# Optimization experiments

Hardware: AMD Instinct MI355X
Metric: run time of the kernel (lower is better)

## Reference

```python
import jax, jax.numpy as jnp
import numpy as np

B, T, C_IN = 2, 4096, 1024
INTER, OUT = 1024, 1024
ROPE_DIM = 64
GAMMA = 0.99609375  # 1 - 2**-8
GROUPS = 32
EPS = 1e-6


def setup_inputs() -> dict:
    key = jax.random.key(0)
    k = jax.random.split(key, 4)
    return {
        "X_Q": jax.random.normal(k[0], (B, T, C_IN), dtype=jnp.float32),
        "W_Q": jax.random.normal(k[1], (C_IN, INTER), dtype=jnp.float32) / C_IN,
        "W_K": jax.random.normal(k[2], (C_IN, INTER), dtype=jnp.float32) / C_IN,
        "W_V": jax.random.normal(k[3], (C_IN, OUT), dtype=jnp.float32) / C_IN,
        "gn_weight": jnp.ones((OUT,), dtype=jnp.float32),
        "gn_bias": jnp.zeros((OUT,), dtype=jnp.float32),
    }


def _rope(x):
    # lucidrains RotaryEmbedding: rotate first ROPE_DIM features, pairwise-adjacent
    t = x.shape[-2]
    inv_freq = 1.0 / (10000.0 ** (jnp.arange(0, ROPE_DIM, 2, dtype=jnp.float32) / ROPE_DIM))
    freqs = jnp.arange(t, dtype=jnp.float32)[:, None] * inv_freq[None, :]  # [T, ROPE_DIM/2]
    freqs = jnp.repeat(freqs, 2, axis=-1)                                   # [T, ROPE_DIM]
    cos, sin = jnp.cos(freqs), jnp.sin(freqs)
    xr, xp = x[..., :ROPE_DIM], x[..., ROPE_DIM:]
    x1, x2 = xr[..., 0::2], xr[..., 1::2]
    rot = jnp.stack([-x2, x1], axis=-1).reshape(xr.shape)  # rotate_half (adjacent pairs)
    return jnp.concatenate([xr * cos + rot * sin, xp], axis=-1)


def _group_norm(x, w, b):
    # torch GroupNorm applied on x.reshape(-1, C)
    sh = x.shape
    c = sh[-1]
    xr = x.reshape(-1, GROUPS, c // GROUPS)
    mu = xr.mean(-1, keepdims=True)
    var = xr.var(-1, keepdims=True)
    xn = ((xr - mu) * jax.lax.rsqrt(var + EPS)).reshape(-1, c)
    return (xn * w + b).reshape(sh)


def reference(X_Q, W_Q, W_K, W_V, gn_weight, gn_bias):
    Q = jax.nn.silu(_rope(X_Q @ W_Q))  # [B,T,INTER]
    K = jax.nn.silu(_rope(X_Q @ W_K))
    V = jax.nn.silu(X_Q @ W_V)         # [B,T,OUT]
    A = jnp.einsum('btd,bsd->bts', Q, K)  # [B,T,T]
    # decay mask: original multiplies by _get_D(gamma,T).T -> gamma^(m-n) for m>=n
    n = jnp.arange(T)[:, None]
    m = jnp.arange(T)[None, :]
    upper = m >= n
    Dt = jnp.where(upper, GAMMA ** jnp.where(upper, m - n, 0).astype(jnp.float32), 0.0)
    A = A * Dt
    out = jnp.einsum('bts,bsd->btd', A, V)  # [B,T,OUT]
    # dropout p=0 (eval) -> identity
    return _group_norm(out, gn_weight, gn_bias)
```

## Files before the change

### kernel.cpp

```cpp
#include <hip/hip_runtime.h>


typedef __attribute__((ext_vector_type(8))) short bf16x8;
typedef __attribute__((ext_vector_type(4))) short bf16x4;
typedef __attribute__((ext_vector_type(4))) float f32x4;

#define MFMA16(a, b, c) __builtin_amdgcn_mfma_f32_16x16x32_bf16(a, b, c, 0, 0, 0)

static __device__ __forceinline__ short f2bf(float f) {
  unsigned u = __builtin_bit_cast(unsigned, f);
  u = (u + 0x7fffu + ((u >> 16) & 1u)) >> 16;
  return (short)u;
}

static __device__ __forceinline__ void gl_lds16(const void* g, void* l) {
  __builtin_amdgcn_global_load_lds(
      (const __attribute__((address_space(1))) void*)g,
      (__attribute__((address_space(3))) void*)l, 16, 0, 0);
}

static __device__ __forceinline__ int swzc(int col, int row) {
  return (((col >> 3) ^ (row & 7)) << 3) | (col & 7);
}

#define T_LEN 4096
#define CIN 1024

#define LOG2G (-0.0056465633f)
#define L2IF (0.41524101f)

__global__ __launch_bounds__(256)
void convert_x(const float* __restrict__ X, short* __restrict__ Xb) {
  const int gid = blockIdx.x * 256 + threadIdx.x;
  const int row = gid >> 7;
  const int c = gid & 127;
  const float* s = &X[(size_t)gid * 8];
  float4 f0 = *(const float4*)s;
  float4 f1 = *(const float4*)(s + 4);
  bf16x8 v = {f2bf(f0.x), f2bf(f0.y), f2bf(f0.z), f2bf(f0.w),
              f2bf(f1.x), f2bf(f1.y), f2bf(f1.z), f2bf(f1.w)};
  const int pc = (c & 0x78) | ((c ^ row) & 7);
  *(bf16x8*)&Xb[(size_t)row * 1024 + pc * 8] = v;
}

__global__ __launch_bounds__(256)
void transpose_w(const float* __restrict__ Wq, const float* __restrict__ Wk,
                 const float* __restrict__ Wv, short* __restrict__ WT) {
  const int k0 = blockIdx.x * 64, n0 = blockIdx.y * 64, mat = blockIdx.z;
  const float* __restrict__ W = (mat == 0) ? Wq : (mat == 1) ? Wk : Wv;
  __shared__ short tile[64][72];
  const int tid = threadIdx.x;
  const int r = tid >> 4, c = tid & 15;
#pragma unroll
  for (int i = 0; i < 4; ++i) {
    int row = r + 16 * i;
    float4 f = *(const float4*)&W[(size_t)(k0 + row) * CIN + n0 + c * 4];
    tile[c * 4 + 0][row] = f2bf(f.x);
    tile[c * 4 + 1][row] = f2bf(f.y);
    tile[c * 4 + 2][row] = f2bf(f.z);
    tile[c * 4 + 3][row] = f2bf(f.w);
  }
  __syncthreads();
  const int n = tid >> 2, seg = tid & 3;
  bf16x8 lo = *(const bf16x8*)&tile[n][seg * 16];
  bf16x8 hi = *(const bf16x8*)&tile[n][seg * 16 + 8];
  const int R = mat * 1024 + n0 + n;
  const int a0 = (k0 >> 3) + seg * 2;
  short* base = &WT[(size_t)R * CIN];
  *(bf16x8*)&base[(a0 ^ (n & 7)) * 8] = lo;
  *(bf16x8*)&base[((a0 + 1) ^ (n & 7)) * 8] = hi;
}

#define GEMM_DECLS()                                   \
  const int tid = threadIdx.x;                         \
  const int lane = tid & 63, wave = tid >> 6;          \
  const int wm = wave >> 1, wn = wave & 1;             \
  const int l15 = lane & 15, quad = lane >> 4;         \
  const int srow = tid >> 3;                           \
  const int scol = (tid & 7) * 8;                      \
  const int asw = (l15 & 7);

#define ACC_INIT4(acc)                                 \
  _Pragma("unroll") for (int i = 0; i < 4; ++i)        \
  _Pragma("unroll") for (int j = 0; j < 4; ++j) {      \
    f32x4 z = {0.f, 0.f, 0.f, 0.f};                    \
    acc[i][j] = z;                                     \
  }

#define STAGE_TILE(dst, src, ld, r0, k0, nrows)        \
  _Pragma("unroll") for (int i = 0; i < (nrows) / 32; ++i) \
    gl_lds16(&src[(size_t)((r0) + i * 32 + srow) * (ld) + (k0) + scol], \
             &dst[i * 32 + srow][scol]);

#define FRAG_MFMA44(As, Bs, acc)                                            \
  {                                                                         \
    bf16x8 af[4][2], bfr[4][2];                                             \
    _Pragma("unroll") for (int im = 0; im < 4; ++im)                        \
    _Pragma("unroll") for (int ks = 0; ks < 2; ++ks)                        \
      af[im][ks] = *(const bf16x8*)&As[wm * 64 + im * 16 + l15]             \
                       [((ks * 4 + quad) ^ asw) * 8];                       \
    _Pragma("unroll") for (int in = 0; in < 4; ++in)                        \
    _Pragma("unroll") for (int ks = 0; ks < 2; ++ks)                        \
      bfr[in][ks] = *(const bf16x8*)&Bs[wn * 64 + in * 16 + l15]            \
                        [((ks * 4 + quad) ^ asw) * 8];                      \
    _Pragma("unroll") for (int ks = 0; ks < 2; ++ks)                        \
    _Pragma("unroll") for (int im = 0; im < 4; ++im)                        \
    _Pragma("unroll") for (int in = 0; in < 4; ++in)                        \
      acc[im][in] = MFMA16(af[im][ks], bfr[in][ks], acc[im][in]);           \
  }

__global__ __launch_bounds__(256, 2)
void qkv_gemm(const short* __restrict__ Xb, const short* __restrict__ WT,
              short* __restrict__ Qb, short* __restrict__ Kb,
              short* __restrict__ Vt) {
  __shared__ __align__(16) short As[128][64];
  __shared__ __align__(16) short Bs[128][64];
  GEMM_DECLS();
  const int m0 = blockIdx.x * 128;
  const int c0 = blockIdx.y * 128;

  f32x4 acc[4][4];
  ACC_INIT4(acc);

  for (int k0 = 0; k0 < CIN; k0 += 64) {
    __syncthreads();
    STAGE_TILE(As, Xb, CIN, m0, k0, 128);
    STAGE_TILE(Bs, WT, CIN, c0, k0, 128);
    __syncthreads();
    FRAG_MFMA44(As, Bs, acc);
  }

  const int mat = (c0 >> 10);
#pragma unroll
  for (int im = 0; im < 4; ++im) {
#pragma unroll
    for (int in = 0; in < 4; ++in) {
      const int c = c0 + wn * 64 + in * 16 + l15;
      const int colm = c & 1023;
      const bool rope = (mat < 2) && (colm < 64);
      const float invf = exp2f(-L2IF * (float)(colm >> 1));
      const int mbase = m0 + wm * 64 + im * 16 + quad * 4;
      short vv[4];
#pragma unroll
      for (int r = 0; r < 4; ++r) {
        float v = acc[im][in][r];
        int m = mbase + r;
        int t = m & (T_LEN - 1);
        float partner = __shfl_xor(v, 1, 64);
        if (rope) {
          float ang = (float)t * invf;
          float s_, c_;
          sincosf(ang, &s_, &c_);
          v = (colm & 1) ? (v * c_ + partner * s_) : (v * c_ - partner * s_);
        }
        v = v / (1.f + __expf(-v));
        vv[r] = f2bf(v);
      }
      if (mat == 0) {
#pragma unroll
        for (int r = 0; r < 4; ++r)
          Qb[(size_t)(mbase + r) * 1024 + swzc(colm, mbase + r)] = vv[r];
      } else if (mat == 1) {
#pragma unroll
        for (int r = 0; r < 4; ++r)
          Kb[(size_t)(mbase + r) * 1024 + swzc(colm, mbase + r)] = vv[r];
      } else {
        bf16x4 v4 = {vv[0], vv[1], vv[2], vv[3]};
        *(bf16x4*)&Vt[(size_t)colm * 8192 +
                      (((mbase >> 3) ^ (colm & 7)) << 3) + (mbase & 7)] = v4;
      }
    }
  }
}

__global__ __launch_bounds__(256, 2)
void score_kernel(const short* __restrict__ Qb, const short* __restrict__ Kb,
                  short* __restrict__ Ab) {
  int idx = blockIdx.x;
  int ti = 0;
  while (idx >= 32 - ti) { idx -= 32 - ti; ++ti; }
  const int si = ti + idx;
  const int b = blockIdx.y;
  const int s0 = si * 128, t0 = ti * 128;

  __shared__ __align__(16) short Qs[128][64];
  __shared__ __align__(16) short Ks[128][64];
  GEMM_DECLS();

  f32x4 acc[4][4];
  ACC_INIT4(acc);

  for (int k0 = 0; k0 < 1024; k0 += 64) {
    __syncthreads();
    STAGE_TILE(Qs, Qb, 1024, b * T_LEN + t0, k0, 128);
    STAGE_TILE(Ks, Kb, 1024, b * T_LEN + s0, k0, 128);
    __syncthreads();
    FRAG_MFMA44(Qs, Ks, acc);
  }

#pragma unroll
  for (int im = 0; im < 4; ++im) {
#pragma unroll
    for (int in = 0; in < 4; ++in) {
      int s = s0 + wn * 64 + in * 16 + l15;
#pragma unroll
      for (int r = 0; r < 4; ++r) {
        int t = t0 + wm * 64 + im * 16 + quad * 4 + r;
        int d = s - t;
        float v = acc[im][in][r];
        v = (d < 0) ? 0.f : v * exp2f((float)d * LOG2G);
        Ab[((size_t)(b * T_LEN + t)) * T_LEN + swzc(s, t)] = f2bf(v);
      }
    }
  }
}

__global__ __launch_bounds__(256, 2)
void av_kernel(const short* __restrict__ Ab, const short* __restrict__ Vt,
               float* __restrict__ Out) {
  const int p = blockIdx.x, b = blockIdx.y, di = blockIdx.z;
  const int n0 = di * 128;

  __shared__ __align__(16) short As2[64][64];
  __shared__ __align__(16) short Vs[128][64];
  GEMM_DECLS();

#pragma unroll 1
  for (int half = 0; half < 2; ++half) {
    const int ti2 = half ? (63 - p) : p;
    const int t0 = ti2 * 64;

    f32x4 acc[2][4];
#pragma unroll
    for (int i = 0; i < 2; ++i)
#pragma unroll
      for (int j = 0; j < 4; ++j) {
        f32x4 z = {0.f, 0.f, 0.f, 0.f};
        acc[i][j] = z;
      }

    for (int s = t0; s < T_LEN; s += 64) {
      __syncthreads();
      STAGE_TILE(As2, Ab, T_LEN, b * T_LEN + t0, s, 64);
      STAGE_TILE(Vs, Vt, 8192, n0, b * T_LEN + s, 128);
      __syncthreads();
      bf16x8 af[2][2], bfr[4][2];
#pragma unroll
      for (int im = 0; im < 2; ++im)
#pragma unroll
        for (int ks = 0; ks < 2; ++ks)
          af[im][ks] = *(const bf16x8*)&As2[wm * 32 + im * 16 + l15]
                           [((ks * 4 + quad) ^ asw) * 8];
#pragma unroll
      for (int in = 0; in < 4; ++in)
#pragma unroll
        for (int ks = 0; ks < 2; ++ks)
          bfr[in][ks] = *(const bf16x8*)&Vs[wn * 64 + in * 16 + l15]
                            [((ks * 4 + quad) ^ asw) * 8];
#pragma unroll
      for (int ks = 0; ks < 2; ++ks)
#pragma unroll
        for (int im = 0; im < 2; ++im)
#pragma unroll
          for (int in = 0; in < 4; ++in)
            acc[im][in] = MFMA16(af[im][ks], bfr[in][ks], acc[im][in]);
    }

#pragma unroll
    for (int im = 0; im < 2; ++im) {
#pragma unroll
      for (int in = 0; in < 4; ++in) {
        int n = n0 + wn * 64 + in * 16 + l15;
#pragma unroll
        for (int r = 0; r < 4; ++r) {
          int t = t0 + wm * 32 + im * 16 + quad * 4 + r;
          Out[((size_t)(b * T_LEN + t)) * 1024 + n] = acc[im][in][r];
        }
      }
    }
  }
}

__global__ __launch_bounds__(256)
void gn_kernel(float* __restrict__ Out, const float* __restrict__ gw,
               const float* __restrict__ gb) {
  const int row = blockIdx.x;
  const int tid = threadIdx.x;
  const int ch0 = tid * 4;
  float4 v = *(const float4*)&Out[(size_t)row * 1024 + ch0];
  float s = v.x + v.y + v.z + v.w;
  float q = v.x * v.x + v.y * v.y + v.z * v.z + v.w * v.w;
  s += __shfl_xor(s, 1, 64);
  q += __shfl_xor(q, 1, 64);
  s += __shfl_xor(s, 2, 64);
  q += __shfl_xor(q, 2, 64);
  s += __shfl_xor(s, 4, 64);
  q += __shfl_xor(q, 4, 64);
  float mean = s * (1.f / 32.f);
  float var = q * (1.f / 32.f) - mean * mean;
  float rstd = rsqrtf(var + 1e-6f);
  float4 o;
  o.x = (v.x - mean) * rstd * gw[ch0 + 0] + gb[ch0 + 0];
  o.y = (v.y - mean) * rstd * gw[ch0 + 1] + gb[ch0 + 1];
  o.z = (v.z - mean) * rstd * gw[ch0 + 2] + gb[ch0 + 2];
  o.w = (v.w - mean) * rstd * gw[ch0 + 3] + gb[ch0 + 3];
  *(float4*)&Out[(size_t)row * 1024 + ch0] = o;
}

extern "C" void kernel_launch(void* const* d_in, const int* in_sizes, int n_in,
                              void* d_out, int out_size, void* d_ws,
                              size_t ws_size, hipStream_t stream) {
  const float* X = (const float*)d_in[0];
  const float* Wq = (const float*)d_in[1];
  const float* Wk = (const float*)d_in[2];
  const float* Wv = (const float*)d_in[3];
  const float* gw = (const float*)d_in[4];
  const float* gb = (const float*)d_in[5];
  float* Out = (float*)d_out;

  short* Qb = (short*)d_ws;
  short* Kb = Qb + (size_t)8192 * 1024;
  short* Vt = Kb + (size_t)8192 * 1024;
  short* Ab = Vt + (size_t)8192 * 1024;
  short* Xb = Ab;
  short* WT = Xb + (size_t)8192 * 1024;

  convert_x<<<4096, 256, 0, stream>>>(X, Xb);
  transpose_w<<<dim3(16, 16, 3), 256, 0, stream>>>(Wq, Wk, Wv, WT);
  qkv_gemm<<<dim3(64, 24), 256, 0, stream>>>(Xb, WT, Qb, Kb, Vt);
  score_kernel<<<dim3(528, 2), 256, 0, stream>>>(Qb, Kb, Ab);
  av_kernel<<<dim3(32, 2, 8), 256, 0, stream>>>(Ab, Vt, Out);
  gn_kernel<<<8192, 256, 0, stream>>>(Out, gw, gb);
}
```

Before: 318.5 us.

## Double-buffer LDS tiles in GEMM kernels and merge prep kernels

```diff
diff --git a/kernel.cpp b/kernel.cpp
--- a/kernel.cpp
+++ b/kernel.cpp
@@ -30,26 +30,28 @@
 #define L2IF (0.41524101f)
 
 __global__ __launch_bounds__(256)
-void convert_x(const float* __restrict__ X, short* __restrict__ Xb) {
-  const int gid = blockIdx.x * 256 + threadIdx.x;
-  const int row = gid >> 7;
-  const int c = gid & 127;
-  const float* s = &X[(size_t)gid * 8];
-  float4 f0 = *(const float4*)s;
-  float4 f1 = *(const float4*)(s + 4);
-  bf16x8 v = {f2bf(f0.x), f2bf(f0.y), f2bf(f0.z), f2bf(f0.w),
-              f2bf(f1.x), f2bf(f1.y), f2bf(f1.z), f2bf(f1.w)};
-  const int pc = (c & 0x78) | ((c ^ row) & 7);
-  *(bf16x8*)&Xb[(size_t)row * 1024 + pc * 8] = v;
-}
-
-__global__ __launch_bounds__(256)
-void transpose_w(const float* __restrict__ Wq, const float* __restrict__ Wk,
+void prep_kernel(const float* __restrict__ X, short* __restrict__ Xb,
+                 const float* __restrict__ Wq, const float* __restrict__ Wk,
                  const float* __restrict__ Wv, short* __restrict__ WT) {
-  const int k0 = blockIdx.x * 64, n0 = blockIdx.y * 64, mat = blockIdx.z;
+  __shared__ short tile[64][72];
+  const int bx = blockIdx.x;
+  const int tid = threadIdx.x;
+  if (bx < 4096) {
+    const int gid = bx * 256 + tid;
+    const int row = gid >> 7;
+    const int c = gid & 127;
+    const float* s = &X[(size_t)gid * 8];
+    float4 f0 = *(const float4*)s;
+    float4 f1 = *(const float4*)(s + 4);
+    bf16x8 v = {f2bf(f0.x), f2bf(f0.y), f2bf(f0.z), f2bf(f0.w),
+                f2bf(f1.x), f2bf(f1.y), f2bf(f1.z), f2bf(f1.w)};
+    const int pc = (c & 0x78) | ((c ^ row) & 7);
+    *(bf16x8*)&Xb[(size_t)row * 1024 + pc * 8] = v;
+    return;
+  }
+  const int bx2 = bx - 4096;
+  const int k0 = (bx2 & 15) * 64, n0 = ((bx2 >> 4) & 15) * 64, mat = bx2 >> 8;
   const float* __restrict__ W = (mat == 0) ? Wq : (mat == 1) ? Wk : Wv;
-  __shared__ short tile[64][72];
-  const int tid = threadIdx.x;
   const int r = tid >> 4, c = tid & 15;
 #pragma unroll
   for (int i = 0; i < 4; ++i) {
@@ -113,8 +115,8 @@
 void qkv_gemm(const short* __restrict__ Xb, const short* __restrict__ WT,
               short* __restrict__ Qb, short* __restrict__ Kb,
               short* __restrict__ Vt) {
-  __shared__ __align__(16) short As[128][64];
-  __shared__ __align__(16) short Bs[128][64];
+  __shared__ __align__(16) short As[2][128][64];
+  __shared__ __align__(16) short Bs[2][128][64];
   GEMM_DECLS();
   const int m0 = blockIdx.x * 128;
   const int c0 = blockIdx.y * 128;
@@ -122,39 +124,53 @@
   f32x4 acc[4][4];
   ACC_INIT4(acc);
 
-  for (int k0 = 0; k0 < CIN; k0 += 64) {
+  STAGE_TILE(As[0], Xb, CIN, m0, 0, 128);
+  STAGE_TILE(Bs[0], WT, CIN, c0, 0, 128);
+
+#pragma unroll 1
+  for (int j = 0; j < 16; ++j) {
     __syncthreads();
-    STAGE_TILE(As, Xb, CIN, m0, k0, 128);
-    STAGE_TILE(Bs, WT, CIN, c0, k0, 128);
-    __syncthreads();
-    FRAG_MFMA44(As, Bs, acc);
+    if (j + 1 < 16) {
+      const int kn = (j + 1) * 64;
+      const int pn = (j + 1) & 1;
+      STAGE_TILE(As[pn], Xb, CIN, m0, kn, 128);
+      STAGE_TILE(Bs[pn], WT, CIN, c0, kn, 128);
+    }
+    const int p = j & 1;
+    FRAG_MFMA44(As[p], Bs[p], acc);
   }
 
   const int mat = (c0 >> 10);
+  const bool ropeBlk = (mat < 2) && ((c0 & 1023) == 0);
 #pragma unroll
   for (int im = 0; im < 4; ++im) {
 #pragma unroll
     for (int in = 0; in < 4; ++in) {
       const int c = c0 + wn * 64 + in * 16 + l15;
       const int colm = c & 1023;
-      const bool rope = (mat < 2) && (colm < 64);
-      const float invf = exp2f(-L2IF * (float)(colm >> 1));
       const int mbase = m0 + wm * 64 + im * 16 + quad * 4;
       short vv[4];
-#pragma unroll
-      for (int r = 0; r < 4; ++r) {
-        float v = acc[im][in][r];
-        int m = mbase + r;
-        int t = m & (T_LEN - 1);
-        float partner = __shfl_xor(v, 1, 64);
-        if (rope) {
+      if (ropeBlk && colm < 64) {
+        const float invf = exp2f(-L2IF * (float)(colm >> 1));
+#pragma unroll
+        for (int r = 0; r < 4; ++r) {
+          float v = acc[im][in][r];
+          int t = (mbase + r) & (T_LEN - 1);
+          float partner = __shfl_xor(v, 1, 64);
           float ang = (float)t * invf;
           float s_, c_;
           sincosf(ang, &s_, &c_);
           v = (colm & 1) ? (v * c_ + partner * s_) : (v * c_ - partner * s_);
+          v = v / (1.f + __expf(-v));
+          vv[r] = f2bf(v);
         }
-        v = v / (1.f + __expf(-v));
-        vv[r] = f2bf(v);
+      } else {
+#pragma unroll
+        for (int r = 0; r < 4; ++r) {
+          float v = acc[im][in][r];
+          v = v / (1.f + __expf(-v));
+          vv[r] = f2bf(v);
+        }
       }
       if (mat == 0) {
 #pragma unroll
@@ -183,19 +199,27 @@
   const int b = blockIdx.y;
   const int s0 = si * 128, t0 = ti * 128;
 
-  __shared__ __align__(16) short Qs[128][64];
-  __shared__ __align__(16) short Ks[128][64];
+  __shared__ __align__(16) short Qs[2][128][64];
+  __shared__ __align__(16) short Ks[2][128][64];
   GEMM_DECLS();
 
   f32x4 acc[4][4];
   ACC_INIT4(acc);
 
-  for (int k0 = 0; k0 < 1024; k0 += 64) {
+  STAGE_TILE(Qs[0], Qb, 1024, b * T_LEN + t0, 0, 128);
+  STAGE_TILE(Ks[0], Kb, 1024, b * T_LEN + s0, 0, 128);
+
+#pragma unroll 1
+  for (int j = 0; j < 16; ++j) {
     __syncthreads();
-    STAGE_TILE(Qs, Qb, 1024, b * T_LEN + t0, k0, 128);
-    STAGE_TILE(Ks, Kb, 1024, b * T_LEN + s0, k0, 128);
-    __syncthreads();
-    FRAG_MFMA44(Qs, Ks, acc);
+    if (j + 1 < 16) {
+      const int kn = (j + 1) * 64;
+      const int pn = (j + 1) & 1;
+      STAGE_TILE(Qs[pn], Qb, 1024, b * T_LEN + t0, kn, 128);
+      STAGE_TILE(Ks[pn], Kb, 1024, b * T_LEN + s0, kn, 128);
+    }
+    const int p = j & 1;
+    FRAG_MFMA44(Qs[p], Ks[p], acc);
   }
 
 #pragma unroll
@@ -220,62 +244,81 @@
                float* __restrict__ Out) {
   const int p = blockIdx.x, b = blockIdx.y, di = blockIdx.z;
   const int n0 = di * 128;
-
-  __shared__ __align__(16) short As2[64][64];
-  __shared__ __align__(16) short Vs[128][64];
+  const int t0a = p * 64, t0b = (63 - p) * 64;
+  const int nA = 64 - p;
+
+  __shared__ __align__(16) short As2[2][64][64];
+  __shared__ __align__(16) short Vs[2][128][64];
   GEMM_DECLS();
 
+  f32x4 accA[2][4], accB[2][4];
+#pragma unroll
+  for (int i = 0; i < 2; ++i)
+#pragma unroll
+    for (int j = 0; j < 4; ++j) {
+      f32x4 z = {0.f, 0.f, 0.f, 0.f};
+      accA[i][j] = z;
+      accB[i][j] = z;
+    }
+
+  STAGE_TILE(As2[0], Ab, T_LEN, b * T_LEN + t0a, t0a, 64);
+  STAGE_TILE(Vs[0], Vt, 8192, n0, b * T_LEN + t0a, 128);
+
 #pragma unroll 1
-  for (int half = 0; half < 2; ++half) {
-    const int ti2 = half ? (63 - p) : p;
-    const int t0 = ti2 * 64;
-
-    f32x4 acc[2][4];
-#pragma unroll
-    for (int i = 0; i < 2; ++i)
-#pragma unroll
-      for (int j = 0; j < 4; ++j) {
-        f32x4 z = {0.f, 0.f, 0.f, 0.f};
-        acc[i][j] = z;
-      }
-
-    for (int s = t0; s < T_LEN; s += 64) {
-      __syncthreads();
-      STAGE_TILE(As2, Ab, T_LEN, b * T_LEN + t0, s, 64);
-      STAGE_TILE(Vs, Vt, 8192, n0, b * T_LEN + s, 128);
-      __syncthreads();
-      bf16x8 af[2][2], bfr[4][2];
-#pragma unroll
-      for (int im = 0; im < 2; ++im)
-#pragma unroll
-        for (int ks = 0; ks < 2; ++ks)
-          af[im][ks] = *(const bf16x8*)&As2[wm * 32 + im * 16 + l15]
-                           [((ks * 4 + quad) ^ asw) * 8];
-#pragma unroll
-      for (int in = 0; in < 4; ++in)
-#pragma unroll
-        for (int ks = 0; ks < 2; ++ks)
-          bfr[in][ks] = *(const bf16x8*)&Vs[wn * 64 + in * 16 + l15]
-                            [((ks * 4 + quad) ^ asw) * 8];
+  for (int j = 0; j < 65; ++j) {
+    __syncthreads();
+    if (j + 1 < 65) {
+      const int jn = j + 1;
+      const int pn = jn & 1;
+      const int tn = (jn < nA) ? t0a : t0b;
+      const int sn = (jn < nA) ? (t0a + 64 * jn) : (t0b + 64 * (jn - nA));
+      STAGE_TILE(As2[pn], Ab, T_LEN, b * T_LEN + tn, sn, 64);
+      STAGE_TILE(Vs[pn], Vt, 8192, n0, b * T_LEN + sn, 128);
+    }
+    const int pb = j & 1;
+    bf16x8 af[2][2], bfr[4][2];
+#pragma unroll
+    for (int im = 0; im < 2; ++im)
 #pragma unroll
       for (int ks = 0; ks < 2; ++ks)
+        af[im][ks] = *(const bf16x8*)&As2[pb][wm * 32 + im * 16 + l15]
+                         [((ks * 4 + quad) ^ asw) * 8];
+#pragma unroll
+    for (int in = 0; in < 4; ++in)
+#pragma unroll
+      for (int ks = 0; ks < 2; ++ks)
+        bfr[in][ks] = *(const bf16x8*)&Vs[pb][wn * 64 + in * 16 + l15]
+                          [((ks * 4 + quad) ^ asw) * 8];
+    if (j < nA) {
+#pragma unroll
+      for (int ks = 0; ks < 2; ++ks)
 #pragma unroll
         for (int im = 0; im < 2; ++im)
 #pragma unroll
           for (int in = 0; in < 4; ++in)
-            acc[im][in] = MFMA16(af[im][ks], bfr[in][ks], acc[im][in]);
-    }
-
-#pragma unroll
-    for (int im = 0; im < 2; ++im) {
-#pragma unroll
-      for (int in = 0; in < 4; ++in) {
-        int n = n0 + wn * 64 + in * 16 + l15;
-#pragma unroll
-        for (int r = 0; r < 4; ++r) {
-          int t = t0 + wm * 32 + im * 16 + quad * 4 + r;
-          Out[((size_t)(b * T_LEN + t)) * 1024 + n] = acc[im][in][r];
-        }
+            accA[im][in] = MFMA16(af[im][ks], bfr[in][ks], accA[im][in]);
+    } else {
+#pragma unroll
+      for (int ks = 0; ks < 2; ++ks)
+#pragma unroll
+        for (int im = 0; im < 2; ++im)
+#pragma unroll
+          for (int in = 0; in < 4; ++in)
+            accB[im][in] = MFMA16(af[im][ks], bfr[in][ks], accB[im][in]);
+    }
+  }
+
+#pragma unroll
+  for (int im = 0; im < 2; ++im) {
+#pragma unroll
+    for (int in = 0; in < 4; ++in) {
+      int n = n0 + wn * 64 + in * 16 + l15;
+#pragma unroll
+      for (int r = 0; r < 4; ++r) {
+        int ta = t0a + wm * 32 + im * 16 + quad * 4 + r;
+        int tb = t0b + wm * 32 + im * 16 + quad * 4 + r;
+        Out[((size_t)(b * T_LEN + ta)) * 1024 + n] = accA[im][in][r];
+        Out[((size_t)(b * T_LEN + tb)) * 1024 + n] = accB[im][in][r];
       }
     }
   }
@@ -325,8 +368,7 @@
   short* Xb = Ab;
   short* WT = Xb + (size_t)8192 * 1024;
 
-  convert_x<<<4096, 256, 0, stream>>>(X, Xb);
-  transpose_w<<<dim3(16, 16, 3), 256, 0, stream>>>(Wq, Wk, Wv, WT);
+  prep_kernel<<<4864, 256, 0, stream>>>(X, Xb, Wq, Wk, Wv, WT);
   qkv_gemm<<<dim3(64, 24), 256, 0, stream>>>(Xb, WT, Qb, Kb, Vt);
   score_kernel<<<dim3(528, 2), 256, 0, stream>>>(Qb, Kb, Ab);
   av_kernel<<<dim3(32, 2, 8), 256, 0, stream>>>(Ab, Vt, Out);
```

New measurement: 334.1 us. 1.05x slower.
